# Optimization experiments

Measured on AMD Instinct MI355X. Metric: run time of the kernel, lower is better.

The kernel has to match this reference:

```python
import jax, jax.numpy as jnp
import numpy as np

N_NODES = 50000
N_EDGES = 800000
IN_DIM = 128
E_FEATS = 64
H = 8
D = IN_DIM // H
NEG_SLOPE = 0.2


def setup_inputs() -> dict:
    key = jax.random.key(0)
    ks = jax.random.split(key, 9)
    h = jax.random.normal(ks[0], (N_NODES, IN_DIM), dtype=jnp.float32)
    edge_features = jax.random.normal(ks[1], (N_EDGES, E_FEATS), dtype=jnp.float32)
    src = jax.random.randint(ks[2], (N_EDGES,), 0, N_NODES, dtype=jnp.int32)
    dst = jax.random.randint(ks[3], (N_EDGES,), 0, N_NODES, dtype=jnp.int32)
    s = 0.05
    Wq = jax.random.normal(ks[4], (IN_DIM, IN_DIM), dtype=jnp.float32) * s
    Wk = jax.random.normal(ks[5], (IN_DIM, IN_DIM), dtype=jnp.float32) * s
    Wv = jax.random.normal(ks[6], (IN_DIM, IN_DIM), dtype=jnp.float32) * s
    We = jax.random.normal(ks[7], (H, E_FEATS), dtype=jnp.float32) * s
    Wres = jax.random.normal(ks[8], (IN_DIM, IN_DIM), dtype=jnp.float32) * s
    return {"h": h, "edge_features": edge_features, "src": src, "dst": dst,
            "Wq": Wq, "Wk": Wk, "Wv": Wv, "We": We, "Wres": Wres}


def reference(h, edge_features, src, dst, Wq, Wk, Wv, We, Wres):
    N = h.shape[0]
    # QKV projections (feat_drop is identity at eval)
    q = (h @ Wq.T).reshape(N, H, D)
    k = (h @ Wk.T).reshape(N, H, D)
    v = (h @ Wv.T).reshape(N, H, D)
    # ee / m_att are computed in the original forward but never used (dead code)
    _ee = edge_features @ We.T  # [E, H]

    # v_dot_u('q','k'): dot(q[dst], k[src]) per edge, per head -> [E, H]
    e = jnp.einsum('ehd,ehd->eh', q[dst], k[src])
    e = jnp.where(e >= 0, e, NEG_SLOPE * e)  # leaky_relu

    # edge_softmax over incoming edges of each destination node
    m = jax.ops.segment_max(e, dst, num_segments=N)          # [N, H]
    ex = jnp.exp(e - m[dst])                                 # [E, H]
    z = jax.ops.segment_sum(ex, dst, num_segments=N)         # [N, H]
    alpha = ex / z[dst]                                      # [E, H] (attn_drop identity)

    # weighted aggregation: sum_e alpha * v[src]
    msg = v[src] * alpha[:, :, None]                         # [E, H, D]
    rst = jax.ops.segment_sum(msg, dst, num_segments=N)      # [N, H, D]
    rst = rst.reshape(N, H * D)
    rst = rst + h @ Wres.T                                   # residual
    return rst
```

## Files before the change

kernel.cpp:

```cpp
#include <hip/hip_runtime.h>


#define NEG_SLOPE 0.2f
#define CB 1024

typedef __attribute__((ext_vector_type(8))) short short8;
typedef __attribute__((ext_vector_type(4))) float f32x4;

__device__ __forceinline__ unsigned short f2bf(float f) {
    unsigned int u = __builtin_bit_cast(unsigned int, f);
    u = (u + 0x7fffu + ((u >> 16) & 1u)) >> 16;
    return (unsigned short)u;
}
__device__ __forceinline__ float bf2f(unsigned short s) {
    unsigned int u = (unsigned int)s << 16;
    return __builtin_bit_cast(float, u);
}

__global__ __launch_bounds__(256) void zero_wconv_kernel(
    const float* __restrict__ Wq, const float* __restrict__ Wk,
    const float* __restrict__ Wv, const float* __restrict__ Wres,
    unsigned short* __restrict__ wpk, int* __restrict__ cnt, int n4)
{
    int t = blockIdx.x * 256 + threadIdx.x;
    if (t < 8192) {
        int l = t & 63;
        int v = t >> 6;
        int kk = v & 3;
        int wct = v >> 2;
        int ct = wct & 7;
        int w = wct >> 3;
        const float* W = (w == 0) ? Wq : (w == 1) ? Wk : (w == 2) ? Wv : Wres;
        const float* srcp = W + (size_t)(ct * 16 + (l & 15)) * 128 + kk * 32 + (l >> 4) * 8;
        float4 lo = *reinterpret_cast<const float4*>(srcp);
        float4 hi = *reinterpret_cast<const float4*>(srcp + 4);
        short8 o;
        o[0] = (short)f2bf(lo.x); o[1] = (short)f2bf(lo.y);
        o[2] = (short)f2bf(lo.z); o[3] = (short)f2bf(lo.w);
        o[4] = (short)f2bf(hi.x); o[5] = (short)f2bf(hi.y);
        o[6] = (short)f2bf(hi.z); o[7] = (short)f2bf(hi.w);
        *reinterpret_cast<short8*>(wpk + (size_t)t * 8) = o;
    } else {
        int u = t - 8192;
        if (u < n4) reinterpret_cast<int4*>(cnt)[u] = make_int4(0, 0, 0, 0);
    }
}

__global__ __launch_bounds__(256) void proj_count_kernel(
    const float* __restrict__ h,
    const unsigned short* __restrict__ wpk,
    unsigned short* __restrict__ qb, unsigned short* __restrict__ kvb,
    float* __restrict__ res,
    const int* __restrict__ dst, int* __restrict__ cnt,
    int N, int E, int PB)
{
    if (blockIdx.x >= PB) {
        int start = (blockIdx.x - PB) * 256 + threadIdx.x;
        for (int e = start; e < E; e += CB * 256)
            atomicAdd(&cnt[dst[e]], 1);
        return;
    }

    const int wid = threadIdx.x >> 6;
    const int lane = threadIdx.x & 63;
    const int row0 = blockIdx.x * 128 + wid * 32;
    const int r = lane & 15, g = lane >> 4;

    short8 afrag[2][4];
    #pragma unroll
    for (int grp = 0; grp < 2; ++grp) {
        int arow = row0 + grp * 16 + r;
        if (arow >= N) arow = N - 1;
        const float* hrow = h + (size_t)arow * 128 + g * 8;
        #pragma unroll
        for (int kk = 0; kk < 4; ++kk) {
            float4 lo = *reinterpret_cast<const float4*>(hrow + kk * 32);
            float4 hi = *reinterpret_cast<const float4*>(hrow + kk * 32 + 4);
            short8 a;
            a[0] = (short)f2bf(lo.x); a[1] = (short)f2bf(lo.y);
            a[2] = (short)f2bf(lo.z); a[3] = (short)f2bf(lo.w);
            a[4] = (short)f2bf(hi.x); a[5] = (short)f2bf(hi.y);
            a[6] = (short)f2bf(hi.z); a[7] = (short)f2bf(hi.w);
            afrag[grp][kk] = a;
        }
    }

    for (int w = 0; w < 4; ++w) {
        f32x4 acc[2][8];
        #pragma unroll
        for (int grp = 0; grp < 2; ++grp)
            #pragma unroll
            for (int ct = 0; ct < 8; ++ct) acc[grp][ct] = (f32x4)(0.f);

        #pragma unroll
        for (int ct = 0; ct < 8; ++ct) {
            const unsigned short* bp =
                wpk + ((size_t)((w * 8 + ct) * 4) * 64 + lane) * 8;
            short8 bfrag[4];
            #pragma unroll
            for (int kk = 0; kk < 4; ++kk)
                bfrag[kk] = *reinterpret_cast<const short8*>(bp + (size_t)kk * 512);
            #pragma unroll
            for (int grp = 0; grp < 2; ++grp)
                #pragma unroll
                for (int kk = 0; kk < 4; ++kk)
                    acc[grp][ct] = __builtin_amdgcn_mfma_f32_16x16x32_bf16(
                        afrag[grp][kk], bfrag[kk], acc[grp][ct], 0, 0, 0);
        }

        #pragma unroll
        for (int grp = 0; grp < 2; ++grp) {
            #pragma unroll
            for (int j = 0; j < 4; ++j) {
                int orow = row0 + grp * 16 + g * 4 + j;
                if (orow < N) {
                    if (w == 0) {
                        #pragma unroll
                        for (int ct = 0; ct < 8; ++ct)
                            qb[(size_t)orow * 128 + ct * 16 + r] = f2bf(acc[grp][ct][j]);
                    } else if (w == 3) {
                        #pragma unroll
                        for (int ct = 0; ct < 8; ++ct)
                            res[(size_t)orow * 128 + ct * 16 + r] = acc[grp][ct][j];
                    } else {
                        const int voff = (w == 2) ? 2 : 0;
                        #pragma unroll
                        for (int ct = 0; ct < 8; ++ct) {
                            int idx = ct * 32 + 4 * (r >> 1) + (r & 1) + voff;
                            kvb[(size_t)orow * 256 + idx] = f2bf(acc[grp][ct][j]);
                        }
                    }
                }
            }
        }
    }
}

__global__ __launch_bounds__(256) void blocksum_kernel(
    const int* __restrict__ cnt, int* __restrict__ bsum, int N)
{
    __shared__ int ws[4];
    const int tid = threadIdx.x;
    int base = blockIdx.x * 1024 + tid * 4;
    int s = 0;
    if (base + 3 < N) {
        int4 v = *reinterpret_cast<const int4*>(cnt + base);
        s = v.x + v.y + v.z + v.w;
    } else {
        for (int i = 0; i < 4; ++i)
            if (base + i < N) s += cnt[base + i];
    }
    #pragma unroll
    for (int m = 32; m >= 1; m >>= 1) s += __shfl_xor(s, m, 64);
    if ((tid & 63) == 0) ws[tid >> 6] = s;
    __syncthreads();
    if (tid == 0) bsum[blockIdx.x] = ws[0] + ws[1] + ws[2] + ws[3];
}

__global__ __launch_bounds__(256) void scanfinal_kernel(
    const int* __restrict__ cnt, const int* __restrict__ bsum,
    int* __restrict__ row_start, int* __restrict__ cursor,
    int N, int E, int NB)
{
    __shared__ int sboff;
    __shared__ int wsum[4];
    const int tid = threadIdx.x, lane = tid & 63, w = tid >> 6;

    if (tid < 64) {
        int v = (tid < NB && tid < blockIdx.x) ? bsum[tid] : 0;
        #pragma unroll
        for (int m = 32; m >= 1; m >>= 1) v += __shfl_xor(v, m, 64);
        if (tid == 0) sboff = v;
    }
    __syncthreads();

    int base = blockIdx.x * 1024 + tid * 4;
    int a0 = 0, a1 = 0, a2 = 0, a3 = 0;
    if (base + 3 < N) {
        int4 v = *reinterpret_cast<const int4*>(cnt + base);
        a0 = v.x; a1 = v.y; a2 = v.z; a3 = v.w;
    } else {
        if (base + 0 < N) a0 = cnt[base + 0];
        if (base + 1 < N) a1 = cnt[base + 1];
        if (base + 2 < N) a2 = cnt[base + 2];
        if (base + 3 < N) a3 = cnt[base + 3];
    }
    const int tsum = a0 + a1 + a2 + a3;
    int v = tsum;
    #pragma unroll
    for (int off = 1; off < 64; off <<= 1) {
        int t = __shfl_up(v, off, 64);
        if (lane >= off) v += t;
    }
    if (lane == 63) wsum[w] = v;
    __syncthreads();
    int woff = 0;
    for (int i = 0; i < w; ++i) woff += wsum[i];
    int run = sboff + woff + v - tsum;

    int r0 = run, r1 = run + a0, r2 = r1 + a1, r3 = r2 + a2;
    if (base + 3 < N) {
        int4 o = make_int4(r0, r1, r2, r3);
        *reinterpret_cast<int4*>(row_start + base) = o;
        *reinterpret_cast<int4*>(cursor + base) = o;
    } else {
        int rr[4] = {r0, r1, r2, r3};
        for (int i = 0; i < 4; ++i)
            if (base + i < N) { row_start[base + i] = rr[i]; cursor[base + i] = rr[i]; }
    }
    if (blockIdx.x == 0 && tid == 0) row_start[N] = E;
}

__global__ __launch_bounds__(256) void scatter_kernel(
    const int* __restrict__ src, const int* __restrict__ dst,
    int* __restrict__ cursor, int* __restrict__ csr_src, int E)
{
    int e = blockIdx.x * 256 + threadIdx.x;
    if (e < E) {
        int d = dst[e];
        int pos = atomicAdd(&cursor[d], 1);
        csr_src[pos] = src[e];
    }
}

__global__ __launch_bounds__(256) void fused_agg_kernel(
    const unsigned short* __restrict__ qb,
    const unsigned short* __restrict__ kvb,
    const int* __restrict__ row_start, const int* __restrict__ csr_src,
    float* __restrict__ rst, int N)
{
    const int lane = threadIdx.x & 63;
    const int node = blockIdx.x * 4 + (threadIdx.x >> 6);
    if (node >= N) return;

    const int beg = row_start[node];
    const int end = row_start[node + 1];
    const int nE = end - beg;
    const int* cp = csr_src + beg;

    ushort2 qraw = *reinterpret_cast<const ushort2*>(qb + (size_t)node * 128 + 2 * lane);
    const float qx = bf2f(qraw.x), qy = bf2f(qraw.y);

    float acc0 = 0.f, acc1 = 0.f, z = 0.f;

    int i = 0;
    int sa = (nE > 0) ? cp[0] : 0;
    int sb = (nE > 1) ? cp[1] : 0;

    while (i + 2 <= nE) {
        const int s0 = sa, s1 = sb;
        i += 2;
        if (i < nE)     sa = cp[i];
        if (i + 1 < nE) sb = cp[i + 1];

        ushort4 kv0 = *reinterpret_cast<const ushort4*>(kvb + (size_t)s0 * 256 + 4 * lane);
        ushort4 kv1 = *reinterpret_cast<const ushort4*>(kvb + (size_t)s1 * 256 + 4 * lane);

        float pA = qx * bf2f(kv0.x) + qy * bf2f(kv0.y);
        float pB = qx * bf2f(kv1.x) + qy * bf2f(kv1.y);
        #pragma unroll
        for (int m = 4; m >= 1; m >>= 1) {
            pA += __shfl_xor(pA, m, 64);
            pB += __shfl_xor(pB, m, 64);
        }
        float e0 = (pA >= 0.f) ? pA : NEG_SLOPE * pA;
        float e1 = (pB >= 0.f) ? pB : NEG_SLOPE * pB;
        e0 = __expf(e0);
        e1 = __expf(e1);
        z += e0 + e1;
        acc0 = fmaf(e0, bf2f(kv0.z), acc0);
        acc1 = fmaf(e0, bf2f(kv0.w), acc1);
        acc0 = fmaf(e1, bf2f(kv1.z), acc0);
        acc1 = fmaf(e1, bf2f(kv1.w), acc1);
    }
    if (i < nE) {
        ushort4 kv0 = *reinterpret_cast<const ushort4*>(kvb + (size_t)sa * 256 + 4 * lane);
        float pA = qx * bf2f(kv0.x) + qy * bf2f(kv0.y);
        #pragma unroll
        for (int m = 4; m >= 1; m >>= 1) pA += __shfl_xor(pA, m, 64);
        float e0 = (pA >= 0.f) ? pA : NEG_SLOPE * pA;
        e0 = __expf(e0);
        z += e0;
        acc0 = fmaf(e0, bf2f(kv0.z), acc0);
        acc1 = fmaf(e0, bf2f(kv0.w), acc1);
    }

    const size_t base = (size_t)node * 128 + 2 * lane;
    float2 rv = *reinterpret_cast<const float2*>(rst + base);
    if (nE > 0) {
        float inv = 1.f / z;
        rv.x = fmaf(acc0, inv, rv.x);
        rv.y = fmaf(acc1, inv, rv.y);
    }
    *reinterpret_cast<float2*>(rst + base) = rv;
}

extern "C" void kernel_launch(void* const* d_in, const int* in_sizes, int n_in,
                              void* d_out, int out_size, void* d_ws, size_t ws_size,
                              hipStream_t stream) {
    const float* h    = (const float*)d_in[0];
    const int*   src  = (const int*)d_in[2];
    const int*   dst  = (const int*)d_in[3];
    const float* Wq   = (const float*)d_in[4];
    const float* Wk   = (const float*)d_in[5];
    const float* Wv   = (const float*)d_in[6];
    const float* Wres = (const float*)d_in[8];
    float* rst = (float*)d_out;

    const int N = in_sizes[0] / 128;
    const int E = in_sizes[2];

    unsigned short* qb  = (unsigned short*)d_ws;
    unsigned short* kvb = qb + (size_t)N * 128;
    unsigned short* wpk = kvb + (size_t)N * 256;
    int* cnt       = (int*)(wpk + 4 * 16384);
    int* row_start = cnt + N;
    int* cursor    = row_start + (N + 1);
    int* csr_src   = cursor + N;
    int* bsum      = csr_src + E;

    const int n4 = N / 4;
    const int NB = (N + 1023) / 1024;
    const int PB = (N + 127) / 128;

    zero_wconv_kernel<<<(8192 + n4 + 255) / 256, 256, 0, stream>>>(
        Wq, Wk, Wv, Wres, wpk, cnt, n4);
    proj_count_kernel<<<PB + CB, 256, 0, stream>>>(h, wpk, qb, kvb, rst,
                                                   dst, cnt, N, E, PB);
    blocksum_kernel<<<NB, 256, 0, stream>>>(cnt, bsum, N);
    scanfinal_kernel<<<NB, 256, 0, stream>>>(cnt, bsum, row_start, cursor,
                                             N, E, NB);
    scatter_kernel<<<(E + 255) / 256, 256, 0, stream>>>(src, dst, cursor,
                                                        csr_src, E);
    fused_agg_kernel<<<(N + 3) / 4, 256, 0, stream>>>(qb, kvb, row_start,
                                                      csr_src, rst, N);
}
```

Before: 170.1 us.

## Split wavefront into two edge streams with 16-byte interleaved K/V loads

Changes the K/V buffer layout so each lane holds 4 interleaved k/v pairs (8 bf16), letting 32 lanes cover a full row with one 16-byte load. The wavefront is split into two halves that each process alternate edges of the same destination node. Their partial sums are then combined with a cross-half shuffle, and only one half writes the output. This is meant to raise memory-level parallelism and halve the shuffle depth per edge, at the cost of masked work on odd edge counts and an extra reduction step.

```diff
diff --git a/kernel.cpp b/kernel.cpp
--- a/kernel.cpp
+++ b/kernel.cpp
@@ -123,10 +123,10 @@
                         for (int ct = 0; ct < 8; ++ct)
                             res[(size_t)orow * 128 + ct * 16 + r] = acc[grp][ct][j];
                     } else {
-                        const int voff = (w == 2) ? 2 : 0;
+                        const int voff = (w == 2) ? 1 : 0;
                         #pragma unroll
                         for (int ct = 0; ct < 8; ++ct) {
-                            int idx = ct * 32 + 4 * (r >> 1) + (r & 1) + voff;
+                            int idx = ct * 32 + 2 * r + voff;
                             kvb[(size_t)orow * 256 + idx] = f2bf(acc[grp][ct][j]);
                         }
                     }
@@ -230,69 +230,67 @@
     float* __restrict__ rst, int N)
 {
     const int lane = threadIdx.x & 63;
+    const int j = lane & 31;
+    const int half = lane >> 5;
     const int node = blockIdx.x * 4 + (threadIdx.x >> 6);
     if (node >= N) return;
 
     const int beg = row_start[node];
-    const int end = row_start[node + 1];
-    const int nE = end - beg;
+    const int nE  = row_start[node + 1] - beg;
+    if (nE <= 0) return;
     const int* cp = csr_src + beg;
-
-    ushort2 qraw = *reinterpret_cast<const ushort2*>(qb + (size_t)node * 128 + 2 * lane);
-    const float qx = bf2f(qraw.x), qy = bf2f(qraw.y);
-
-    float acc0 = 0.f, acc1 = 0.f, z = 0.f;
-
-    int i = 0;
-    int sa = (nE > 0) ? cp[0] : 0;
-    int sb = (nE > 1) ? cp[1] : 0;
-
-    while (i + 2 <= nE) {
-        const int s0 = sa, s1 = sb;
-        i += 2;
-        if (i < nE)     sa = cp[i];
-        if (i + 1 < nE) sb = cp[i + 1];
-
-        ushort4 kv0 = *reinterpret_cast<const ushort4*>(kvb + (size_t)s0 * 256 + 4 * lane);
-        ushort4 kv1 = *reinterpret_cast<const ushort4*>(kvb + (size_t)s1 * 256 + 4 * lane);
-
-        float pA = qx * bf2f(kv0.x) + qy * bf2f(kv0.y);
-        float pB = qx * bf2f(kv1.x) + qy * bf2f(kv1.y);
-        #pragma unroll
-        for (int m = 4; m >= 1; m >>= 1) {
-            pA += __shfl_xor(pA, m, 64);
-            pB += __shfl_xor(pB, m, 64);
-        }
-        float e0 = (pA >= 0.f) ? pA : NEG_SLOPE * pA;
-        float e1 = (pB >= 0.f) ? pB : NEG_SLOPE * pB;
-        e0 = __expf(e0);
-        e1 = __expf(e1);
-        z += e0 + e1;
-        acc0 = fmaf(e0, bf2f(kv0.z), acc0);
-        acc1 = fmaf(e0, bf2f(kv0.w), acc1);
-        acc0 = fmaf(e1, bf2f(kv1.z), acc0);
-        acc1 = fmaf(e1, bf2f(kv1.w), acc1);
-    }
-    if (i < nE) {
-        ushort4 kv0 = *reinterpret_cast<const ushort4*>(kvb + (size_t)sa * 256 + 4 * lane);
-        float pA = qx * bf2f(kv0.x) + qy * bf2f(kv0.y);
-        #pragma unroll
-        for (int m = 4; m >= 1; m >>= 1) pA += __shfl_xor(pA, m, 64);
-        float e0 = (pA >= 0.f) ? pA : NEG_SLOPE * pA;
-        e0 = __expf(e0);
-        z += e0;
-        acc0 = fmaf(e0, bf2f(kv0.z), acc0);
-        acc1 = fmaf(e0, bf2f(kv0.w), acc1);
-    }
-
-    const size_t base = (size_t)node * 128 + 2 * lane;
-    float2 rv = *reinterpret_cast<const float2*>(rst + base);
-    if (nE > 0) {
+    const int last = nE - 1;
+
+    ushort4 qraw = *reinterpret_cast<const ushort4*>(qb + (size_t)node * 128 + 4 * j);
+    const float q0 = bf2f(qraw.x), q1 = bf2f(qraw.y),
+                q2 = bf2f(qraw.z), q3 = bf2f(qraw.w);
+
+    float a0 = 0.f, a1 = 0.f, a2 = 0.f, a3 = 0.f, z = 0.f;
+
+    int sa = cp[min(half, last)];
+    int sb = cp[min(half + 2, last)];
+
+    #pragma unroll 2
+    for (int i = 0; i < nE; i += 2) {
+        const int ii = i + half;
+        const float m = (ii < nE) ? 1.f : 0.f;
+        const int scur = sa;
+        sa = sb;
+        sb = cp[min(ii + 4, last)];
+
+        const unsigned short* kp = kvb + (size_t)scur * 256 + 8 * j;
+        short8 kv8 = *reinterpret_cast<const short8*>(kp);
+        float p = q0 * bf2f((unsigned short)kv8[0])
+                + q1 * bf2f((unsigned short)kv8[2])
+                + q2 * bf2f((unsigned short)kv8[4])
+                + q3 * bf2f((unsigned short)kv8[6]);
+        p += __shfl_xor(p, 1, 64);
+        p += __shfl_xor(p, 2, 64);
+        float e = (p >= 0.f) ? p : NEG_SLOPE * p;
+        e = m * __expf(e);
+        z += e;
+        a0 = fmaf(e, bf2f((unsigned short)kv8[1]), a0);
+        a1 = fmaf(e, bf2f((unsigned short)kv8[3]), a1);
+        a2 = fmaf(e, bf2f((unsigned short)kv8[5]), a2);
+        a3 = fmaf(e, bf2f((unsigned short)kv8[7]), a3);
+    }
+
+    a0 += __shfl_xor(a0, 32, 64);
+    a1 += __shfl_xor(a1, 32, 64);
+    a2 += __shfl_xor(a2, 32, 64);
+    a3 += __shfl_xor(a3, 32, 64);
+    z  += __shfl_xor(z, 32, 64);
+
+    if (half == 0) {
+        const size_t base = (size_t)node * 128 + 4 * j;
         float inv = 1.f / z;
-        rv.x = fmaf(acc0, inv, rv.x);
-        rv.y = fmaf(acc1, inv, rv.y);
-    }
-    *reinterpret_cast<float2*>(rst + base) = rv;
+        float4 rv = *reinterpret_cast<const float4*>(rst + base);
+        rv.x = fmaf(a0, inv, rv.x);
+        rv.y = fmaf(a1, inv, rv.y);
+        rv.z = fmaf(a2, inv, rv.z);
+        rv.w = fmaf(a3, inv, rv.w);
+        *reinterpret_cast<float4*>(rst + base) = rv;
+    }
 }
 
 extern "C" void kernel_launch(void* const* d_in, const int* in_sizes, int n_in,
```

Measured after the change: 173.8 us. 2.2% more time.
